# Performance work log

Hardware: AMD Instinct MI355X
Metric: run time of the kernel (lower is better)

## Reference

```python
import jax, jax.numpy as jnp
import numpy as np

NB_STEPS = 50
ALPHA = 0.9
NUM_RNN_STEPS = 2
B = 4096
NUM_FEATURE = 100
IN_D = 5
HIDDEN = [64, 64, 64]
P1 = (1.1, 1.1, 1.5, 2.0, 2.5)   # IntegrandNN_outer_level powers
P2 = (1.5, 2.0, 2.5, 3.0, 3.5)   # IntegrandNN powers


def _cc(nb_steps):
    # Clenshaw-Curtis weights/steps, identical to UMNN's compute_cc_weights
    n = nb_steps
    i = np.arange(n + 1, dtype=np.float64).reshape(-1, 1)
    lam = np.cos(i @ i.T * np.pi / n)
    lam[:, 0] = 0.5
    lam[:, -1] *= 0.5
    lam = lam * 2.0 / n
    W = np.zeros(n + 1)
    even = np.arange(0, n + 1, 2)
    W[even] = 2.0 / (1.0 - even.astype(np.float64) ** 2)
    W[0] = 1.0
    ccw = (lam.T @ W).astype(np.float32)                         # [n+1]
    steps = np.cos(np.arange(n + 1) * np.pi / n).astype(np.float32)  # [n+1]
    return jnp.asarray(ccw), jnp.asarray(steps)

CC_W, CC_S = _cc(NB_STEPS)


def _mlp(xh, Ws, bs):
    # Linear+ReLU stack with ELU on the last layer (ReLU popped, ELU appended)
    h = xh
    for W, b in zip(Ws[:-1], bs[:-1]):
        h = jax.nn.relu(h @ W.T + b)
    return jax.nn.elu(h @ Ws[-1].T + bs[-1])


def _integrand(x, h, Ws, bs, Wf, powers):
    z = _mlp(jnp.concatenate([x, h], axis=1), Ws, bs) + 1.0      # [N,1], z >= 0
    feats = jnp.concatenate([z ** p for p in powers], axis=1)    # [N,5]
    return jax.nn.relu((1.0 / (feats + 1.0)) @ Wf.T)             # [N,1]


def _integrate(x0, xT, h, f):
    # ParallelNeuralIntegral forward: CC quadrature of f from x0 to xT
    Bn, S = x0.shape[0], NB_STEPS + 1
    X = x0[:, None, :] + (xT - x0)[:, None, :] * (CC_S[None, :, None] + 1.0) / 2.0  # [B,S,1]
    hs = jnp.broadcast_to(h[:, None, :], (Bn, S, h.shape[1])).reshape(-1, h.shape[1])
    dz = f(X.reshape(-1, 1), hs).reshape(Bn, S, 1)
    return (dz * CC_W[None, :, None]).sum(1) * (xT - x0) / 2.0   # [B,1]


def setup_inputs() -> dict:
    key = jax.random.key(0)
    ks = jax.random.split(key, 24)
    def lin(k, o, i):
        return jax.random.normal(k, (o, i), jnp.float32) / np.sqrt(i)
    d = {}
    d["x_"] = jax.random.normal(ks[0], (B, NUM_FEATURE), jnp.float32)
    d["h_"] = jax.random.normal(ks[1], (B, IN_D - 1), jnp.float32)
    d["log_weight"] = jnp.ones((1, NUM_FEATURE), jnp.float32)     # reset_parameters -> 1
    d["sigmoid_param"] = jnp.zeros((1,), jnp.float32)
    sizes = [IN_D] + HIDDEN + [1]
    for tag, base in (("f1", 2), ("f2", 12)):
        for li, (i, o) in enumerate(zip(sizes[:-1], sizes[1:])):
            d[f"{tag}_W{li}"] = lin(ks[base + 2 * li], o, i)
            d[f"{tag}_b{li}"] = jnp.zeros((o,), jnp.float32)
        d[f"{tag}_Wf"] = jnp.abs(lin(ks[base + 9], 1, 5))         # reset_params -> abs
    return d


def reference(x_, h_, log_weight, sigmoid_param,
              f1_W0, f1_b0, f1_W1, f1_b1, f1_W2, f1_b2, f1_W3, f1_b3, f1_Wf,
              f2_W0, f2_b0, f2_W1, f2_b1, f2_W2, f2_b2, f2_W3, f2_b3, f2_Wf):
    f1Ws = [f1_W0, f1_W1, f1_W2, f1_W3]; f1bs = [f1_b0, f1_b1, f1_b2, f1_b3]
    f2Ws = [f2_W0, f2_W1, f2_W2, f2_W3]; f2bs = [f2_b0, f2_b1, f2_b2, f2_b3]
    f1 = lambda x, h: _integrand(x, h, f1Ws, f1bs, f1_Wf, P1)
    f2 = lambda x, h: _integrand(x, h, f2Ws, f2bs, f2_Wf, P2)

    # modular function: linear to [B,1] then sum over dim 1 -> [B,1]
    xm = jnp.sum(x_ * log_weight[0], axis=1, keepdims=True)
    lam = jax.nn.sigmoid(sigmoid_param[0])

    I1 = jnp.zeros_like(xm)
    I2 = jnp.zeros_like(xm)
    out_first = None
    for _ in range(NUM_RNN_STEPS):
        x = (1.0 - lam) * xm + lam * I1
        x2 = (1.0 - lam) * xm + lam * I2
        out_first = f1(x2, h_)
        I1 = _integrate(jnp.zeros_like(x), x, h_, f1)
        xmax = jnp.max(x2) + 10.0
        xfinal = jnp.zeros_like(x) + xmax
        I2 = (1.0 / ALPHA) * _integrate(x2, xfinal, h_, f2)
    return I1, out_first, I2
```

## Files before the change

### kernel.cpp

```cpp
#include <hip/hip_runtime.h>
#include <math.h>

typedef _Float16 half8v __attribute__((ext_vector_type(8)));
typedef _Float16 half4v __attribute__((ext_vector_type(4)));
typedef _Float16 half2v __attribute__((ext_vector_type(2)));
typedef float float4v __attribute__((ext_vector_type(4)));

#define BB    4096
#define NS    51
#define TBR   5
#define NBI   820
#define NBF   16
#define GRID_INT (2*NBI + NBF)
#define INV_ALPHA (1.0f/0.9f)
#define AROW  72

#define WS_CCW  0
#define WS_CCS  64
#define WS_LAM  128
#define WS_PM16 160
#define WS_PM64 192
#define WS_XM   256
#define WS_X    (WS_XM + BB)
#define WS_X2   (WS_X + BB)
#define WS_H    12544
#define H_NET   8192
#define H_W2    4096
#define H_W0    16384
#define H_W3    20480

__global__ void k_setup(const float* __restrict__ x_, const float* __restrict__ lw,
                        const float* __restrict__ sp,
                        const float* __restrict__ f1W0, const float* __restrict__ f1W1,
                        const float* __restrict__ f1W2, const float* __restrict__ f1W3,
                        const float* __restrict__ f2W0, const float* __restrict__ f2W1,
                        const float* __restrict__ f2W2, const float* __restrict__ f2W3,
                        float* __restrict__ ws) {
    _Float16* wh = (_Float16*)(ws + WS_H);
    const int blk = blockIdx.x, tid = threadIdx.x;
    if (blk < 64) {
        int wave = tid >> 6, lane = tid & 63;
        float vmax = -1e30f;
        for (int r = 0; r < 16; ++r) {
            int row = blk * 64 + wave * 16 + r;
            float v = 0.0f;
            for (int i = lane; i < 100; i += 64) v = fmaf(x_[row * 100 + i], lw[i], v);
            #pragma unroll
            for (int off = 32; off > 0; off >>= 1) v += __shfl_xor(v, off, 64);
            if (lane == 0) ws[WS_XM + row] = v;
            vmax = fmaxf(vmax, v);
        }
        __shared__ float sm[4];
        if (lane == 0) sm[wave] = vmax;
        __syncthreads();
        if (tid == 0)
            ws[WS_PM64 + blk] = fmaxf(fmaxf(sm[0], sm[1]), fmaxf(sm[2], sm[3]));
    } else if (blk < 80) {
        int t = (blk - 64) * 256 + tid;
        wh[t]               = (_Float16)f1W1[t];
        wh[H_W2 + t]        = (_Float16)f1W2[t];
        wh[H_NET + t]       = (_Float16)f2W1[t];
        wh[H_NET + H_W2 + t] = (_Float16)f2W2[t];
        if (t < 2048) {
            int j = t >> 5, k = t & 31;
            wh[H_W0 + t]        = (k < 5) ? (_Float16)f1W0[j * 5 + k] : (_Float16)0.0f;
            wh[H_W0 + 2048 + t] = (k < 5) ? (_Float16)f2W0[j * 5 + k] : (_Float16)0.0f;
        }
        if (t < 64) {
            wh[H_W3 + t]      = (_Float16)f1W3[t];
            wh[H_W3 + 64 + t] = (_Float16)f2W3[t];
        }
    } else {
        if (tid == 60) ws[WS_LAM] = 1.0f / (1.0f + expf(-sp[0]));
        if (tid <= 50) {
            ws[WS_CCS + tid] = cospif((float)tid / 50.0f);
            float acc = 0.0f;
            for (int a = 0; a <= 50; ++a) {
                float w;
                if (a == 0) w = 1.0f;
                else if ((a & 1) == 0) w = 2.0f / (1.0f - (float)(a * a));
                else continue;
                float l;
                if (tid == 0) l = 0.5f;
                else {
                    int m = (a * tid) % 100;
                    l = cospif((float)m / 50.0f);
                    if (tid == 50) l *= 0.5f;
                }
                acc += l * 0.04f * w;
            }
            ws[WS_CCW + tid] = acc;
        }
    }
}

__global__ void k_pre(const float* __restrict__ xm, const float* __restrict__ out,
                      const float* __restrict__ ws_lam,
                      float* __restrict__ x, float* __restrict__ x2,
                      float* __restrict__ pmax) {
    int b = blockIdx.x * 256 + threadIdx.x;
    float lam = ws_lam[0];
    float m = xm[b];
    float xv  = (1.0f - lam) * m + lam * out[b];
    float x2v = (1.0f - lam) * m + lam * out[2 * BB + b];
    x[b] = xv;
    x2[b] = x2v;
    __shared__ float red[256];
    red[threadIdx.x] = x2v;
    __syncthreads();
    #pragma unroll
    for (int off = 128; off > 0; off >>= 1) {
        if (threadIdx.x < off)
            red[threadIdx.x] = fmaxf(red[threadIdx.x], red[threadIdx.x + off]);
        __syncthreads();
    }
    if (threadIdx.x == 0) pmax[blockIdx.x] = red[0];
}

__device__ __forceinline__ void mfma_hidden(
    const _Float16* __restrict__ Wg, const float* __restrict__ Bg,
    _Float16* act, int tid)
{
    const int lane = tid & 63, wbase = tid & 192;
    const int lo = lane & 15, quad = lane >> 4;
    half8v Af[4][2];
    #pragma unroll
    for (int m = 0; m < 4; ++m)
        #pragma unroll
        for (int kb = 0; kb < 2; ++kb)
            Af[m][kb] = *(const half8v*)(Wg + (16 * m + lo) * 64 + 32 * kb + quad * 8);
    float4v bb[4];
    #pragma unroll
    for (int m = 0; m < 4; ++m) bb[m] = *(const float4v*)(Bg + 16 * m + quad * 4);
    half8v Bf[4][2];
    #pragma unroll
    for (int n = 0; n < 4; ++n)
        #pragma unroll
        for (int kb = 0; kb < 2; ++kb)
            Bf[n][kb] = *(const half8v*)(act + (wbase + 16 * n + lo) * AROW + 32 * kb + quad * 8);
    float4v accv[4][4];
    #pragma unroll
    for (int m = 0; m < 4; ++m)
        #pragma unroll
        for (int n = 0; n < 4; ++n) {
            float4v c = bb[m];
            c = __builtin_amdgcn_mfma_f32_16x16x32_f16(Af[m][0], Bf[n][0], c, 0, 0, 0);
            c = __builtin_amdgcn_mfma_f32_16x16x32_f16(Af[m][1], Bf[n][1], c, 0, 0, 0);
            accv[m][n] = c;
        }
    #pragma unroll
    for (int m = 0; m < 4; ++m)
        #pragma unroll
        for (int n = 0; n < 4; ++n) {
            float4v c = accv[m][n];
            half4v o;
            o[0] = (_Float16)fmaxf(c[0], 0.0f); o[1] = (_Float16)fmaxf(c[1], 0.0f);
            o[2] = (_Float16)fmaxf(c[2], 0.0f); o[3] = (_Float16)fmaxf(c[3], 0.0f);
            *(half4v*)(act + (wbase + 16 * n + lo) * AROW + 16 * m + quad * 4) = o;
        }
}

__device__ __forceinline__ void mfma_first(
    const _Float16* __restrict__ Wg, const float* __restrict__ Bg,
    _Float16* act, int tid)
{
    const int lane = tid & 63, wbase = tid & 192;
    const int lo = lane & 15, quad = lane >> 4;
    half8v Af[4];
    #pragma unroll
    for (int m = 0; m < 4; ++m)
        Af[m] = *(const half8v*)(Wg + (16 * m + lo) * 32 + quad * 8);
    float4v bb[4];
    #pragma unroll
    for (int m = 0; m < 4; ++m) bb[m] = *(const float4v*)(Bg + 16 * m + quad * 4);
    half8v Bf[4];
    #pragma unroll
    for (int n = 0; n < 4; ++n)
        Bf[n] = *(const half8v*)(act + (wbase + 16 * n + lo) * AROW + quad * 8);
    float4v accv[4][4];
    #pragma unroll
    for (int m = 0; m < 4; ++m)
        #pragma unroll
        for (int n = 0; n < 4; ++n)
            accv[m][n] = __builtin_amdgcn_mfma_f32_16x16x32_f16(Af[m], Bf[n], bb[m], 0, 0, 0);
    #pragma unroll
    for (int m = 0; m < 4; ++m)
        #pragma unroll
        for (int n = 0; n < 4; ++n) {
            float4v c = accv[m][n];
            half4v o;
            o[0] = (_Float16)fmaxf(c[0], 0.0f); o[1] = (_Float16)fmaxf(c[1], 0.0f);
            o[2] = (_Float16)fmaxf(c[2], 0.0f); o[3] = (_Float16)fmaxf(c[3], 0.0f);
            *(half4v*)(act + (wbase + 16 * n + lo) * AROW + 16 * m + quad * 4) = o;
        }
}

__global__ __launch_bounds__(256) void k_int(
    int mode, const float* __restrict__ ws, const float* __restrict__ h_,
    const float* __restrict__ f1b0, const float* __restrict__ f1b1,
    const float* __restrict__ f1b2, const float* __restrict__ f1b3,
    const float* __restrict__ f1Wf,
    const float* __restrict__ f2b0, const float* __restrict__ f2b1,
    const float* __restrict__ f2b2, const float* __restrict__ f2b3,
    const float* __restrict__ f2Wf,
    float* __restrict__ out)
{
    __shared__ _Float16 act[256 * AROW];
    __shared__ float red[256];

    const int blk = blockIdx.x, tid = threadIdx.x;
    const float* xm = ws + WS_XM;
    const float* xarr = ws + WS_X;
    const float* x2arr = ws + WS_X2;
    const _Float16* wh = (const _Float16*)(ws + WS_H);
    const float lam = ws[WS_LAM];
    const float oml = 1.0f - lam;

    int kind, b_base = 0, b, s = 0;
    if (blk < NBI)          { kind = 0; b_base = blk * TBR; }
    else if (blk < 2 * NBI) { kind = 1; b_base = (blk - NBI) * TBR; }
    else                    { kind = 2; }

    float xmax = 0.0f, xin;
    if (kind == 2) {
        b = (blk - 2 * NBI) * 256 + tid;
        xin = mode ? x2arr[b] : oml * xm[b];
    } else {
        if (kind == 1) {
            int lane = tid & 63;
            const float* pm = mode ? (ws + WS_PM16) : (ws + WS_PM64);
            int cnt = mode ? 16 : 64;
            float v = (lane < cnt) ? pm[lane] : -1e30f;
            #pragma unroll
            for (int off = 32; off > 0; off >>= 1) v = fmaxf(v, __shfl_xor(v, off, 64));
            xmax = (mode ? v : oml * v) + 10.0f;
        }
        int lb = tid / 51;
        s = tid - lb * 51;
        b = b_base + (lb < TBR - 1 ? lb : TBR - 1);
        if (b > BB - 1) b = BB - 1;
        float t = (ws[WS_CCS + s] + 1.0f) * 0.5f;
        if (kind == 0) {
            float xb = mode ? xarr[b] : oml * xm[b];
            xin = xb * t;
        } else {
            float x0v = mode ? x2arr[b] : oml * xm[b];
            xin = x0v + (xmax - x0v) * t;
        }
    }
    const float4 h4 = ((const float4*)h_)[b];

    const bool u2 = (kind == 1);
    const _Float16* W0h = wh + H_W0 + (u2 ? 2048 : 0);
    const _Float16* W1h = wh + (u2 ? H_NET : 0);
    const _Float16* W2h = W1h + H_W2;
    const _Float16* W3h = wh + H_W3 + (u2 ? 64 : 0);
    const float* B0 = u2 ? f2b0 : f1b0;
    const float* B1 = u2 ? f2b1 : f1b1;
    const float* B2 = u2 ? f2b2 : f1b2;
    const float* B3 = u2 ? f2b3 : f1b3;
    const float* WF = u2 ? f2Wf : f1Wf;
    const float p0 = u2 ? 1.5f : 1.1f;
    const float p1 = u2 ? 2.0f : 1.1f;
    const float p2 = u2 ? 2.5f : 1.5f;
    const float p3 = u2 ? 3.0f : 2.0f;
    const float p4 = u2 ? 3.5f : 2.5f;

    {
        _Float16* myrow = act + tid * AROW;
        half8v sv;
        sv[0] = (_Float16)xin; sv[1] = (_Float16)h4.x; sv[2] = (_Float16)h4.y;
        sv[3] = (_Float16)h4.z; sv[4] = (_Float16)h4.w;
        sv[5] = (_Float16)0.0f; sv[6] = (_Float16)0.0f; sv[7] = (_Float16)0.0f;
        half8v zv;
        #pragma unroll
        for (int e = 0; e < 8; ++e) zv[e] = (_Float16)0.0f;
        *(half8v*)(myrow)      = sv;
        *(half8v*)(myrow + 8)  = zv;
        *(half8v*)(myrow + 16) = zv;
        *(half8v*)(myrow + 24) = zv;
    }

    mfma_first (W0h, B0, act, tid);
    mfma_hidden(W1h, B1, act, tid);
    mfma_hidden(W2h, B2, act, tid);

    float y = B3[0];
    {
        const _Float16* myrow = act + tid * AROW;
        #pragma unroll
        for (int g = 0; g < 8; ++g) {
            half8v hv = *(const half8v*)(myrow + 8 * g);
            half8v wv = *(const half8v*)(W3h + 8 * g);
            #pragma unroll
            for (int p = 0; p < 4; ++p) {
                half2v a; a[0] = hv[2 * p]; a[1] = hv[2 * p + 1];
                half2v w; w[0] = wv[2 * p]; w[1] = wv[2 * p + 1];
#if defined(__has_builtin) && __has_builtin(__builtin_amdgcn_fdot2)
                y = __builtin_amdgcn_fdot2(a, w, y, false);
#else
                y = fmaf((float)a[0], (float)w[0], y);
                y = fmaf((float)a[1], (float)w[1], y);
#endif
            }
        }
    }
    if (y <= 0.0f) y = __expf(y) - 1.0f;
    float z = y + 1.0f;
    float lg = __logf(z);
    float g = WF[0] / (__expf(p0 * lg) + 1.0f)
            + WF[1] / (__expf(p1 * lg) + 1.0f)
            + WF[2] / (__expf(p2 * lg) + 1.0f)
            + WF[3] / (__expf(p3 * lg) + 1.0f)
            + WF[4] / (__expf(p4 * lg) + 1.0f);
    float val = fmaxf(g, 0.0f);

    if (kind == 2) { out[BB + b] = val; return; }

    red[tid] = ws[WS_CCW + s] * val;
    __syncthreads();
    if (tid < TBR) {
        float sum = 0.0f;
        for (int i = 0; i < NS; ++i) sum += red[tid * NS + i];
        int bo = b_base + tid;
        if (bo < BB) {
            if (kind == 0) {
                float xb = mode ? xarr[bo] : oml * xm[bo];
                out[bo] = sum * xb * 0.5f;
            } else {
                float x2b = mode ? x2arr[bo] : oml * xm[bo];
                out[2 * BB + bo] = sum * (xmax - x2b) * 0.5f * INV_ALPHA;
            }
        }
    }
}

extern "C" void kernel_launch(void* const* d_in, const int* in_sizes, int n_in,
                              void* d_out, int out_size, void* d_ws, size_t ws_size,
                              hipStream_t stream) {
    const float* x_  = (const float*)d_in[0];
    const float* h_  = (const float*)d_in[1];
    const float* lw  = (const float*)d_in[2];
    const float* sp  = (const float*)d_in[3];
    const float* f1W0 = (const float*)d_in[4];   const float* f1b0 = (const float*)d_in[5];
    const float* f1W1 = (const float*)d_in[6];   const float* f1b1 = (const float*)d_in[7];
    const float* f1W2 = (const float*)d_in[8];   const float* f1b2 = (const float*)d_in[9];
    const float* f1W3 = (const float*)d_in[10];  const float* f1b3 = (const float*)d_in[11];
    const float* f1Wf = (const float*)d_in[12];
    const float* f2W0 = (const float*)d_in[13];  const float* f2b0 = (const float*)d_in[14];
    const float* f2W1 = (const float*)d_in[15];  const float* f2b1 = (const float*)d_in[16];
    const float* f2W2 = (const float*)d_in[17];  const float* f2b2 = (const float*)d_in[18];
    const float* f2W3 = (const float*)d_in[19];  const float* f2b3 = (const float*)d_in[20];
    const float* f2Wf = (const float*)d_in[21];
    float* out = (float*)d_out;
    float* ws  = (float*)d_ws;

    k_setup<<<81, 256, 0, stream>>>(x_, lw, sp,
                                    f1W0, f1W1, f1W2, f1W3,
                                    f2W0, f2W1, f2W2, f2W3, ws);
    k_int<<<GRID_INT, 256, 0, stream>>>(0, ws, h_,
        f1b0, f1b1, f1b2, f1b3, f1Wf, f2b0, f2b1, f2b2, f2b3, f2Wf, out);
    k_pre<<<16, 256, 0, stream>>>(ws + WS_XM, out, ws + WS_LAM,
                                  ws + WS_X, ws + WS_X2, ws + WS_PM16);
    k_int<<<GRID_INT, 256, 0, stream>>>(1, ws, h_,
        f1b0, f1b1, f1b2, f1b3, f1Wf, f2b0, f2b1, f2b2, f2b3, f2Wf, out);
}
```

Measured before the change: 165.0 us.

## Fuse k_pre into k_int epilogue, swizzle LDS activations, widen setup grid

Drops the k_pre launch. The first integration pass now writes the next x and x2 directly and computes the global max of x2 with an atomicMax on an order-preserving integer key. The padded LDS activation layout (72-half rows) is replaced by an XOR-swizzled 64-half layout, and the reduction buffer is aliased onto it, so an extra barrier is added before reuse. It also spreads the xm reduction over 256 setup blocks, replaces divisions with hardware reciprocal, and replaces fdot2 with scalar fma. These changes remove a kernel launch and cut LDS footprint and bank conflicts, at the cost of an atomic and slightly lower reciprocal precision.

```diff
diff --git a/kernel.cpp b/kernel.cpp
--- a/kernel.cpp
+++ b/kernel.cpp
@@ -3,7 +3,6 @@
 
 typedef _Float16 half8v __attribute__((ext_vector_type(8)));
 typedef _Float16 half4v __attribute__((ext_vector_type(4)));
-typedef _Float16 half2v __attribute__((ext_vector_type(2)));
 typedef float float4v __attribute__((ext_vector_type(4)));
 
 #define BB    4096
@@ -13,21 +12,42 @@
 #define NBF   16
 #define GRID_INT (2*NBI + NBF)
 #define INV_ALPHA (1.0f/0.9f)
-#define AROW  72
-
-#define WS_CCW  0
-#define WS_CCS  64
-#define WS_LAM  128
-#define WS_PM16 160
-#define WS_PM64 192
-#define WS_XM   256
-#define WS_X    (WS_XM + BB)
-#define WS_X2   (WS_X + BB)
-#define WS_H    12544
-#define H_NET   8192
-#define H_W2    4096
-#define H_W0    16384
-#define H_W3    20480
+
+#define WS_CCW 0
+#define WS_CCS 64
+#define WS_LAM 128
+#define WS_KEY 132
+#define WS_PM  144
+#define WS_XM  512
+#define WS_X   (WS_XM + BB)
+#define WS_X2  (WS_X + BB)
+#define WS_H   16384
+#define H_NET  8192
+#define H_W2   4096
+#define H_W0   16384
+#define H_W3   20480
+
+#if defined(__has_builtin)
+#if __has_builtin(__builtin_amdgcn_rcpf)
+#define FRCP(x) __builtin_amdgcn_rcpf(x)
+#endif
+#endif
+#ifndef FRCP
+#define FRCP(x) (1.0f / (x))
+#endif
+
+__device__ __forceinline__ unsigned fkey(float f) {
+    int i = __float_as_int(f);
+    return (i >= 0) ? ((unsigned)i + 0x80000000u) : ~(unsigned)i;
+}
+__device__ __forceinline__ float fkey_inv(unsigned k) {
+    return (k & 0x80000000u) ? __int_as_float((int)(k - 0x80000000u))
+                             : __int_as_float((int)~k);
+}
+
+__device__ __forceinline__ int swz(int row, int cb) {
+    return (row << 6) + (((cb ^ (row & 7)) & 7) << 3);
+}
 
 __global__ void k_setup(const float* __restrict__ x_, const float* __restrict__ lw,
                         const float* __restrict__ sp,
@@ -38,11 +58,11 @@
                         float* __restrict__ ws) {
     _Float16* wh = (_Float16*)(ws + WS_H);
     const int blk = blockIdx.x, tid = threadIdx.x;
-    if (blk < 64) {
+    if (blk < 256) {
         int wave = tid >> 6, lane = tid & 63;
         float vmax = -1e30f;
-        for (int r = 0; r < 16; ++r) {
-            int row = blk * 64 + wave * 16 + r;
+        for (int r = 0; r < 4; ++r) {
+            int row = blk * 16 + wave * 4 + r;
             float v = 0.0f;
             for (int i = lane; i < 100; i += 64) v = fmaf(x_[row * 100 + i], lw[i], v);
             #pragma unroll
@@ -54,12 +74,12 @@
         if (lane == 0) sm[wave] = vmax;
         __syncthreads();
         if (tid == 0)
-            ws[WS_PM64 + blk] = fmaxf(fmaxf(sm[0], sm[1]), fmaxf(sm[2], sm[3]));
-    } else if (blk < 80) {
-        int t = (blk - 64) * 256 + tid;
-        wh[t]               = (_Float16)f1W1[t];
-        wh[H_W2 + t]        = (_Float16)f1W2[t];
-        wh[H_NET + t]       = (_Float16)f2W1[t];
+            ws[WS_PM + blk] = fmaxf(fmaxf(sm[0], sm[1]), fmaxf(sm[2], sm[3]));
+    } else if (blk < 272) {
+        int t = (blk - 256) * 256 + tid;
+        wh[t]                = (_Float16)f1W1[t];
+        wh[H_W2 + t]         = (_Float16)f1W2[t];
+        wh[H_NET + t]        = (_Float16)f2W1[t];
         wh[H_NET + H_W2 + t] = (_Float16)f2W2[t];
         if (t < 2048) {
             int j = t >> 5, k = t & 31;
@@ -72,6 +92,7 @@
         }
     } else {
         if (tid == 60) ws[WS_LAM] = 1.0f / (1.0f + expf(-sp[0]));
+        if (tid == 61) ((unsigned*)ws)[WS_KEY] = 0u;
         if (tid <= 50) {
             ws[WS_CCS + tid] = cospif((float)tid / 50.0f);
             float acc = 0.0f;
@@ -94,29 +115,6 @@
     }
 }
 
-__global__ void k_pre(const float* __restrict__ xm, const float* __restrict__ out,
-                      const float* __restrict__ ws_lam,
-                      float* __restrict__ x, float* __restrict__ x2,
-                      float* __restrict__ pmax) {
-    int b = blockIdx.x * 256 + threadIdx.x;
-    float lam = ws_lam[0];
-    float m = xm[b];
-    float xv  = (1.0f - lam) * m + lam * out[b];
-    float x2v = (1.0f - lam) * m + lam * out[2 * BB + b];
-    x[b] = xv;
-    x2[b] = x2v;
-    __shared__ float red[256];
-    red[threadIdx.x] = x2v;
-    __syncthreads();
-    #pragma unroll
-    for (int off = 128; off > 0; off >>= 1) {
-        if (threadIdx.x < off)
-            red[threadIdx.x] = fmaxf(red[threadIdx.x], red[threadIdx.x + off]);
-        __syncthreads();
-    }
-    if (threadIdx.x == 0) pmax[blockIdx.x] = red[0];
-}
-
 __device__ __forceinline__ void mfma_hidden(
     const _Float16* __restrict__ Wg, const float* __restrict__ Bg,
     _Float16* act, int tid)
@@ -137,7 +135,7 @@
     for (int n = 0; n < 4; ++n)
         #pragma unroll
         for (int kb = 0; kb < 2; ++kb)
-            Bf[n][kb] = *(const half8v*)(act + (wbase + 16 * n + lo) * AROW + 32 * kb + quad * 8);
+            Bf[n][kb] = *(const half8v*)(act + swz(wbase + 16 * n + lo, 4 * kb + quad));
     float4v accv[4][4];
     #pragma unroll
     for (int m = 0; m < 4; ++m)
@@ -156,7 +154,7 @@
             half4v o;
             o[0] = (_Float16)fmaxf(c[0], 0.0f); o[1] = (_Float16)fmaxf(c[1], 0.0f);
             o[2] = (_Float16)fmaxf(c[2], 0.0f); o[3] = (_Float16)fmaxf(c[3], 0.0f);
-            *(half4v*)(act + (wbase + 16 * n + lo) * AROW + 16 * m + quad * 4) = o;
+            *(half4v*)(act + swz(wbase + 16 * n + lo, 2 * m + (quad >> 1)) + 4 * (quad & 1)) = o;
         }
 }
 
@@ -176,7 +174,7 @@
     half8v Bf[4];
     #pragma unroll
     for (int n = 0; n < 4; ++n)
-        Bf[n] = *(const half8v*)(act + (wbase + 16 * n + lo) * AROW + quad * 8);
+        Bf[n] = *(const half8v*)(act + swz(wbase + 16 * n + lo, quad));
     float4v accv[4][4];
     #pragma unroll
     for (int m = 0; m < 4; ++m)
@@ -191,12 +189,12 @@
             half4v o;
             o[0] = (_Float16)fmaxf(c[0], 0.0f); o[1] = (_Float16)fmaxf(c[1], 0.0f);
             o[2] = (_Float16)fmaxf(c[2], 0.0f); o[3] = (_Float16)fmaxf(c[3], 0.0f);
-            *(half4v*)(act + (wbase + 16 * n + lo) * AROW + 16 * m + quad * 4) = o;
+            *(half4v*)(act + swz(wbase + 16 * n + lo, 2 * m + (quad >> 1)) + 4 * (quad & 1)) = o;
         }
 }
 
 __global__ __launch_bounds__(256) void k_int(
-    int mode, const float* __restrict__ ws, const float* __restrict__ h_,
+    int mode, float* __restrict__ ws, const float* __restrict__ h_,
     const float* __restrict__ f1b0, const float* __restrict__ f1b1,
     const float* __restrict__ f1b2, const float* __restrict__ f1b3,
     const float* __restrict__ f1Wf,
@@ -205,8 +203,8 @@
     const float* __restrict__ f2Wf,
     float* __restrict__ out)
 {
-    __shared__ _Float16 act[256 * AROW];
-    __shared__ float red[256];
+    __shared__ _Float16 act[256 * 64];
+    float* red = (float*)act;
 
     const int blk = blockIdx.x, tid = threadIdx.x;
     const float* xm = ws + WS_XM;
@@ -227,13 +225,17 @@
         xin = mode ? x2arr[b] : oml * xm[b];
     } else {
         if (kind == 1) {
-            int lane = tid & 63;
-            const float* pm = mode ? (ws + WS_PM16) : (ws + WS_PM64);
-            int cnt = mode ? 16 : 64;
-            float v = (lane < cnt) ? pm[lane] : -1e30f;
-            #pragma unroll
-            for (int off = 32; off > 0; off >>= 1) v = fmaxf(v, __shfl_xor(v, off, 64));
-            xmax = (mode ? v : oml * v) + 10.0f;
+            if (mode) {
+                xmax = fkey_inv(((const unsigned*)ws)[WS_KEY]) + 10.0f;
+            } else {
+                int lane = tid & 63;
+                const float* pm = ws + WS_PM;
+                float v = fmaxf(fmaxf(pm[lane], pm[lane + 64]),
+                                fmaxf(pm[lane + 128], pm[lane + 192]));
+                #pragma unroll
+                for (int off = 32; off > 0; off >>= 1) v = fmaxf(v, __shfl_xor(v, off, 64));
+                xmax = oml * v + 10.0f;
+            }
         }
         int lb = tid / 51;
         s = tid - lb * 51;
@@ -267,7 +269,6 @@
     const float p4 = u2 ? 3.5f : 2.5f;
 
     {
-        _Float16* myrow = act + tid * AROW;
         half8v sv;
         sv[0] = (_Float16)xin; sv[1] = (_Float16)h4.x; sv[2] = (_Float16)h4.y;
         sv[3] = (_Float16)h4.z; sv[4] = (_Float16)h4.w;
@@ -275,10 +276,10 @@
         half8v zv;
         #pragma unroll
         for (int e = 0; e < 8; ++e) zv[e] = (_Float16)0.0f;
-        *(half8v*)(myrow)      = sv;
-        *(half8v*)(myrow + 8)  = zv;
-        *(half8v*)(myrow + 16) = zv;
-        *(half8v*)(myrow + 24) = zv;
+        *(half8v*)(act + swz(tid, 0)) = sv;
+        *(half8v*)(act + swz(tid, 1)) = zv;
+        *(half8v*)(act + swz(tid, 2)) = zv;
+        *(half8v*)(act + swz(tid, 3)) = zv;
     }
 
     mfma_first (W0h, B0, act, tid);
@@ -286,51 +287,62 @@
     mfma_hidden(W2h, B2, act, tid);
 
     float y = B3[0];
-    {
-        const _Float16* myrow = act + tid * AROW;
-        #pragma unroll
-        for (int g = 0; g < 8; ++g) {
-            half8v hv = *(const half8v*)(myrow + 8 * g);
-            half8v wv = *(const half8v*)(W3h + 8 * g);
-            #pragma unroll
-            for (int p = 0; p < 4; ++p) {
-                half2v a; a[0] = hv[2 * p]; a[1] = hv[2 * p + 1];
-                half2v w; w[0] = wv[2 * p]; w[1] = wv[2 * p + 1];
-#if defined(__has_builtin) && __has_builtin(__builtin_amdgcn_fdot2)
-                y = __builtin_amdgcn_fdot2(a, w, y, false);
-#else
-                y = fmaf((float)a[0], (float)w[0], y);
-                y = fmaf((float)a[1], (float)w[1], y);
-#endif
-            }
-        }
+    #pragma unroll
+    for (int g = 0; g < 8; ++g) {
+        half8v hv = *(const half8v*)(act + swz(tid, g));
+        half8v wv = *(const half8v*)(W3h + 8 * g);
+        #pragma unroll
+        for (int e = 0; e < 8; ++e) y = fmaf((float)wv[e], (float)hv[e], y);
     }
     if (y <= 0.0f) y = __expf(y) - 1.0f;
     float z = y + 1.0f;
     float lg = __logf(z);
-    float g = WF[0] / (__expf(p0 * lg) + 1.0f)
-            + WF[1] / (__expf(p1 * lg) + 1.0f)
-            + WF[2] / (__expf(p2 * lg) + 1.0f)
-            + WF[3] / (__expf(p3 * lg) + 1.0f)
-            + WF[4] / (__expf(p4 * lg) + 1.0f);
+    float g = WF[0] * FRCP(__expf(p0 * lg) + 1.0f)
+            + WF[1] * FRCP(__expf(p1 * lg) + 1.0f)
+            + WF[2] * FRCP(__expf(p2 * lg) + 1.0f)
+            + WF[3] * FRCP(__expf(p3 * lg) + 1.0f)
+            + WF[4] * FRCP(__expf(p4 * lg) + 1.0f);
     float val = fmaxf(g, 0.0f);
 
     if (kind == 2) { out[BB + b] = val; return; }
 
+    __syncthreads();
     red[tid] = ws[WS_CCW + s] * val;
     __syncthreads();
-    if (tid < TBR) {
-        float sum = 0.0f;
-        for (int i = 0; i < NS; ++i) sum += red[tid * NS + i];
-        int bo = b_base + tid;
-        if (bo < BB) {
-            if (kind == 0) {
+
+    if (kind == 0) {
+        if (tid < TBR) {
+            float sum = 0.0f;
+            for (int i = 0; i < NS; ++i) sum += red[tid * NS + i];
+            int bo = b_base + tid;
+            if (bo < BB) {
                 float xb = mode ? xarr[bo] : oml * xm[bo];
-                out[bo] = sum * xb * 0.5f;
-            } else {
+                float I1 = sum * xb * 0.5f;
+                out[bo] = I1;
+                if (!mode) ws[WS_X + bo] = oml * xm[bo] + lam * I1;
+            }
+        }
+    } else {
+        float x2n = -3e38f;
+        if (tid < TBR) {
+            float sum = 0.0f;
+            for (int i = 0; i < NS; ++i) sum += red[tid * NS + i];
+            int bo = b_base + tid;
+            if (bo < BB) {
                 float x2b = mode ? x2arr[bo] : oml * xm[bo];
-                out[2 * BB + bo] = sum * (xmax - x2b) * 0.5f * INV_ALPHA;
+                float I2 = sum * (xmax - x2b) * 0.5f * INV_ALPHA;
+                out[2 * BB + bo] = I2;
+                if (!mode) {
+                    x2n = oml * xm[bo] + lam * I2;
+                    ws[WS_X2 + bo] = x2n;
+                }
             }
+        }
+        if (!mode && tid < 64) {
+            #pragma unroll
+            for (int off = 32; off > 0; off >>= 1)
+                x2n = fmaxf(x2n, __shfl_xor(x2n, off, 64));
+            if (tid == 0) atomicMax((unsigned*)ws + WS_KEY, fkey(x2n));
         }
     }
 }
@@ -355,13 +367,11 @@
     float* out = (float*)d_out;
     float* ws  = (float*)d_ws;
 
-    k_setup<<<81, 256, 0, stream>>>(x_, lw, sp,
-                                    f1W0, f1W1, f1W2, f1W3,
-                                    f2W0, f2W1, f2W2, f2W3, ws);
+    k_setup<<<273, 256, 0, stream>>>(x_, lw, sp,
+                                     f1W0, f1W1, f1W2, f1W3,
+                                     f2W0, f2W1, f2W2, f2W3, ws);
     k_int<<<GRID_INT, 256, 0, stream>>>(0, ws, h_,
         f1b0, f1b1, f1b2, f1b3, f1Wf, f2b0, f2b1, f2b2, f2b3, f2Wf, out);
-    k_pre<<<16, 256, 0, stream>>>(ws + WS_XM, out, ws + WS_LAM,
-                                  ws + WS_X, ws + WS_X2, ws + WS_PM16);
     k_int<<<GRID_INT, 256, 0, stream>>>(1, ws, h_,
         f1b0, f1b1, f1b2, f1b3, f1Wf, f2b0, f2b1, f2b2, f2b3, f2Wf, out);
 }
```

After: 162.6 us. About the same (-1.4%).
